# Optimization experiments

Hardware: AMD Instinct MI355X
Metric: run time of the kernel (lower is better)

The kernel has to match this reference:

```python
import jax, jax.numpy as jnp
import numpy as np

N_NODES = 50000
IN_CH, HID_CH, OUT_CH = 128, 128, 16
N_EDGES = 800000


def setup_inputs() -> dict:
    key = jax.random.key(0)
    ks = jax.random.split(key, 10)
    def lin_w(k, fan_in, fan_out):
        bound = 1.0 / np.sqrt(fan_in)
        return jax.random.uniform(k, (fan_in, fan_out), jnp.float32, -bound, bound)
    inp = {
        'x': jax.random.normal(ks[0], (N_NODES, IN_CH), jnp.float32),
        'edge_index': jax.random.randint(ks[1], (2, N_EDGES), 0, N_NODES, jnp.int64),
        # SAGEConv l/r weights: lin_l (neighbor aggregate, with bias), lin_r (root, no bias)
        'W1_l': lin_w(ks[2], IN_CH, HID_CH), 'b1': jnp.zeros((HID_CH,), jnp.float32),
        'W1_r': lin_w(ks[3], IN_CH, HID_CH),
        'W2_l': lin_w(ks[4], HID_CH, HID_CH), 'b2': jnp.zeros((HID_CH,), jnp.float32),
        'W2_r': lin_w(ks[5], HID_CH, HID_CH),
        'W3_l': lin_w(ks[6], HID_CH, HID_CH), 'b3': jnp.zeros((HID_CH,), jnp.float32),
        'W3_r': lin_w(ks[7], HID_CH, HID_CH),
        'W_lin': lin_w(ks[8], HID_CH, OUT_CH), 'b_lin': jnp.zeros((OUT_CH,), jnp.float32),
    }
    return inp


def _sage_conv(x, src, dst, W_l, b_l, W_r, n_nodes):
    # mean aggregation of source-node features at destination nodes
    msg_sum = jax.ops.segment_sum(x[src], dst, num_segments=n_nodes)  # [N, d]
    deg = jax.ops.segment_sum(jnp.ones((src.shape[0],), x.dtype), dst, num_segments=n_nodes)
    mean = msg_sum / jnp.maximum(deg, 1.0)[:, None]
    return mean @ W_l + b_l + x @ W_r


def reference(x, edge_index, W1_l, b1, W1_r, W2_l, b2, W2_r, W3_l, b3, W3_r, W_lin, b_lin):
    src, dst = edge_index[0], edge_index[1]
    n = x.shape[0]
    h = jax.nn.relu(_sage_conv(x, src, dst, W1_l, b1, W1_r, n))
    h = jax.nn.relu(_sage_conv(h, src, dst, W2_l, b2, W2_r, n))
    # dropout is identity in eval mode
    h = jax.nn.relu(_sage_conv(h, src, dst, W3_l, b3, W3_r, n))
    return h @ W_lin + b_lin
```

## Files before the change

### kernel.cpp

```cpp
#include <hip/hip_runtime.h>


typedef short bf16x8 __attribute__((ext_vector_type(8)));
typedef float f32x4 __attribute__((ext_vector_type(4)));

__device__ __forceinline__ float bf16_to_f32(unsigned int lo16) {
  unsigned int u = lo16 << 16;
  return __builtin_bit_cast(float, u);
}
__device__ __forceinline__ unsigned short f32_to_bf16(float f) {
  unsigned int u = __builtin_bit_cast(unsigned int, f);
  unsigned int r = (u + 0x7FFFu + ((u >> 16) & 1u)) >> 16;
  return (unsigned short)r;
}

__device__ __forceinline__ void gload_lds16(void* g, void* lds_base) {
  __builtin_amdgcn_global_load_lds(
      (__attribute__((address_space(1))) unsigned int*)(uintptr_t)g,
      (__attribute__((address_space(3))) unsigned int*)(unsigned int)(uintptr_t)lds_base,
      16, 0, 0);
}

__global__ void k_zero_i32(int* __restrict__ p, int n) {
  int i = blockIdx.x * blockDim.x + threadIdx.x;
  if (i < n) p[i] = 0;
}

__global__ __launch_bounds__(256) void k_split(const float* __restrict__ in,
                                               unsigned short* __restrict__ hi,
                                               unsigned short* __restrict__ lo, int n4) {
  int i = blockIdx.x * blockDim.x + threadIdx.x;
  if (i < n4) {
    float4 v = *reinterpret_cast<const float4*>(&in[(size_t)i * 4]);
    ushort4 h, l;
    h.x = f32_to_bf16(v.x); l.x = f32_to_bf16(v.x - bf16_to_f32(h.x));
    h.y = f32_to_bf16(v.y); l.y = f32_to_bf16(v.y - bf16_to_f32(h.y));
    h.z = f32_to_bf16(v.z); l.z = f32_to_bf16(v.z - bf16_to_f32(h.z));
    h.w = f32_to_bf16(v.w); l.w = f32_to_bf16(v.w - bf16_to_f32(h.w));
    *reinterpret_cast<ushort4*>(&hi[(size_t)i * 4]) = h;
    *reinterpret_cast<ushort4*>(&lo[(size_t)i * 4]) = l;
  }
}

__global__ __launch_bounds__(256) void k_prep_w(const float* __restrict__ Wl,
                                                const float* __restrict__ Wr,
                                                unsigned short* __restrict__ Whi,
                                                unsigned short* __restrict__ Wlo) {
  int n = blockIdx.x, k = threadIdx.x;
  float v = (k < 128) ? Wl[(size_t)k * 128 + n] : Wr[(size_t)(k - 128) * 128 + n];
  unsigned short h = f32_to_bf16(v);
  Whi[(size_t)n * 256 + k] = h;
  Wlo[(size_t)n * 256 + k] = f32_to_bf16(v - bf16_to_f32(h));
}

__global__ void k_detect(const int* __restrict__ ei, int* __restrict__ flag) {
  int t = threadIdx.x;
  int any = 0;
  for (int i = t; i < 1024; i += 256)
    if (ei[2 * i + 1] != 0) any = 1;
  if (any) atomicOr(flag, 1);
}

__device__ __forceinline__ int load_src(const int* ei, int E, int i, int is32) {
  return is32 ? ei[i] : ei[2 * i];
}
__device__ __forceinline__ int load_dst(const int* ei, int E, int i, int is32) {
  return is32 ? ei[E + i] : ei[2 * E + 2 * i];
}

__global__ __launch_bounds__(256) void k_count(const int* __restrict__ ei,
                                               const int* __restrict__ flag,
                                               int* __restrict__ deg,
                                               int* __restrict__ erank, int E) {
  int i = blockIdx.x * blockDim.x + threadIdx.x;
  if (i < E) {
    int is32 = *flag;
    erank[i] = atomicAdd(&deg[load_dst(ei, E, i, is32)], 1);
  }
}

__global__ __launch_bounds__(256) void k_scan1(const int* __restrict__ deg,
                                               int* __restrict__ bsum, int N) {
  __shared__ int s[256];
  int t = threadIdx.x;
  int base = blockIdx.x * 1024 + t * 4;
  int v = 0;
#pragma unroll
  for (int j = 0; j < 4; ++j) {
    int i = base + j;
    v += (i < N) ? deg[i] : 0;
  }
  s[t] = v;
  __syncthreads();
  for (int off = 128; off > 0; off >>= 1) {
    if (t < off) s[t] += s[t + off];
    __syncthreads();
  }
  if (t == 0) bsum[blockIdx.x] = s[0];
}

__global__ __launch_bounds__(1024) void k_scan2(int* __restrict__ bsum,
                                                int* __restrict__ row_ptr,
                                                int nb, int N) {
  __shared__ int s[1024];
  int t = threadIdx.x;
  int v = (t < nb) ? bsum[t] : 0;
  s[t] = v;
  __syncthreads();
  for (int off = 1; off < 1024; off <<= 1) {
    int add = (t >= off) ? s[t - off] : 0;
    __syncthreads();
    s[t] += add;
    __syncthreads();
  }
  if (t < nb) bsum[t] = s[t] - v;
  if (t == 1023) row_ptr[N] = s[1023];
}

__global__ __launch_bounds__(256) void k_scan3(const int* __restrict__ deg,
                                               const int* __restrict__ bsum,
                                               int* __restrict__ row_ptr,
                                               float* __restrict__ inv_deg, int N) {
  __shared__ int s[256];
  int t = threadIdx.x;
  int base = blockIdx.x * 1024 + t * 4;
  int v[4];
  int sum = 0;
#pragma unroll
  for (int j = 0; j < 4; ++j) {
    int i = base + j;
    v[j] = (i < N) ? deg[i] : 0;
    sum += v[j];
  }
  s[t] = sum;
  __syncthreads();
  for (int off = 1; off < 256; off <<= 1) {
    int add = (t >= off) ? s[t - off] : 0;
    __syncthreads();
    s[t] += add;
    __syncthreads();
  }
  int excl = s[t] - sum + bsum[blockIdx.x];
#pragma unroll
  for (int j = 0; j < 4; ++j) {
    int i = base + j;
    if (i < N) {
      row_ptr[i] = excl;
      inv_deg[i] = 1.0f / (float)((v[j] > 1) ? v[j] : 1);
      excl += v[j];
    }
  }
}

__global__ __launch_bounds__(256) void k_fill(const int* __restrict__ ei,
                                              const int* __restrict__ flag,
                                              const int* __restrict__ row_ptr,
                                              const int* __restrict__ erank,
                                              int* __restrict__ col_idx, int E) {
  int i = blockIdx.x * blockDim.x + threadIdx.x;
  if (i < E) {
    int is32 = *flag;
    int d = load_dst(ei, E, i, is32);
    int s = load_src(ei, E, i, is32);
    col_idx[row_ptr[d] + erank[i]] = s;
  }
}

__global__ __launch_bounds__(256) void k_aggregate(const unsigned short* __restrict__ Xhi,
                                                   const int* __restrict__ row_ptr,
                                                   const int* __restrict__ col_idx,
                                                   const float* __restrict__ inv_deg,
                                                   unsigned int* __restrict__ Mhi,
                                                   unsigned int* __restrict__ Mlo, int N) {
  int gw = (int)((blockIdx.x * blockDim.x + threadIdx.x) >> 6);
  int lane = threadIdx.x & 63;
  if (gw >= N) return;
  int s = row_ptr[gw], e = row_ptr[gw + 1];
  const unsigned int* Xp =
      reinterpret_cast<const unsigned int*>(Xhi) + lane;
  float ax[8], ay[8];
#pragma unroll
  for (int q = 0; q < 8; ++q) { ax[q] = 0.f; ay[q] = 0.f; }
  int j = s;
  for (; j + 8 <= e; j += 8) {
    unsigned int v[8];
#pragma unroll
    for (int q = 0; q < 8; ++q) v[q] = Xp[(size_t)col_idx[j + q] * 64];
#pragma unroll
    for (int q = 0; q < 8; ++q) {
      ax[q] += bf16_to_f32(v[q] & 0xFFFFu);
      ay[q] += bf16_to_f32(v[q] >> 16);
    }
  }
  for (; j + 4 <= e; j += 4) {
    unsigned int v[4];
#pragma unroll
    for (int q = 0; q < 4; ++q) v[q] = Xp[(size_t)col_idx[j + q] * 64];
#pragma unroll
    for (int q = 0; q < 4; ++q) {
      ax[q] += bf16_to_f32(v[q] & 0xFFFFu);
      ay[q] += bf16_to_f32(v[q] >> 16);
    }
  }
  for (; j < e; ++j) {
    unsigned int v = Xp[(size_t)col_idx[j] * 64];
    ax[0] += bf16_to_f32(v & 0xFFFFu);
    ay[0] += bf16_to_f32(v >> 16);
  }
  float inv = inv_deg[gw];
  float rx = ((ax[0] + ax[1]) + (ax[2] + ax[3])) + ((ax[4] + ax[5]) + (ax[6] + ax[7]));
  float ry = ((ay[0] + ay[1]) + (ay[2] + ay[3])) + ((ay[4] + ay[5]) + (ay[6] + ay[7]));
  rx *= inv;
  ry *= inv;
  unsigned int hx = f32_to_bf16(rx), hy = f32_to_bf16(ry);
  unsigned int lx = f32_to_bf16(rx - bf16_to_f32(hx));
  unsigned int ly = f32_to_bf16(ry - bf16_to_f32(hy));
  Mhi[(size_t)gw * 64 + lane] = hx | (hy << 16);
  Mlo[(size_t)gw * 64 + lane] = lx | (ly << 16);
}

__global__ __launch_bounds__(256) void k_mfma_gemm(
    const unsigned short* __restrict__ A1hi, const unsigned short* __restrict__ A1lo,
    const unsigned short* __restrict__ A2hi, const unsigned short* __restrict__ A2lo,
    const unsigned short* __restrict__ Whi, const unsigned short* __restrict__ Wlo,
    const float* __restrict__ bias,
    unsigned short* __restrict__ Ohi, unsigned short* __restrict__ Olo, int N) {
  __shared__ unsigned short sAhi[128 * 32], sAlo[128 * 32];
  __shared__ unsigned short sBhi[128 * 32], sBlo[128 * 32];
  int t = threadIdx.x;
  int lane = t & 63;
  int w = t >> 6;
  int wr = (w >> 1) * 64, wc = (w & 1) * 64;
  int block_row = blockIdx.x * 128;

  f32x4 acc[4][4];
#pragma unroll
  for (int m = 0; m < 4; ++m)
#pragma unroll
    for (int n = 0; n < 4; ++n) acc[m][n] = f32x4{0.f, 0.f, 0.f, 0.f};

  int kg = lane & 3;
  int rr = lane >> 2;
  int fr = lane & 15;
  int fkb = (lane >> 4) * 16;

  for (int kt = 0; kt < 8; ++kt) {
    {
      const unsigned short* gsrc;
      unsigned short* lbase;
      int isA = (w < 2);
      if (w == 0) { gsrc = (kt < 4) ? A1hi : A2hi; lbase = sAhi; }
      else if (w == 1) { gsrc = (kt < 4) ? A1lo : A2lo; lbase = sAlo; }
      else if (w == 2) { gsrc = Whi; lbase = sBhi; }
      else { gsrc = Wlo; lbase = sBlo; }
#pragma unroll
      for (int c = 0; c < 8; ++c) {
        int idx = c * 16 + rr;
        const char* src;
        if (isA) {
          int rg = block_row + idx;
          if (rg > N - 1) rg = N - 1;
          src = (const char*)gsrc + (size_t)rg * 256 + (kt & 3) * 64 + kg * 16;
        } else {
          src = (const char*)gsrc + (size_t)idx * 512 + kt * 64 + kg * 16;
        }
        gload_lds16((void*)src, (char*)lbase + c * 1024);
      }
    }
    __syncthreads();
    bf16x8 a_hi[4], a_lo[4], b_hi[4], b_lo[4];
#pragma unroll
    for (int m = 0; m < 4; ++m) {
      int row = wr + m * 16 + fr;
      a_hi[m] = *reinterpret_cast<const bf16x8*>((const char*)sAhi + row * 64 + fkb);
      a_lo[m] = *reinterpret_cast<const bf16x8*>((const char*)sAlo + row * 64 + fkb);
    }
#pragma unroll
    for (int n = 0; n < 4; ++n) {
      int col = wc + n * 16 + fr;
      b_hi[n] = *reinterpret_cast<const bf16x8*>((const char*)sBhi + col * 64 + fkb);
      b_lo[n] = *reinterpret_cast<const bf16x8*>((const char*)sBlo + col * 64 + fkb);
    }
#pragma unroll
    for (int m = 0; m < 4; ++m)
#pragma unroll
      for (int n = 0; n < 4; ++n) {
        acc[m][n] = __builtin_amdgcn_mfma_f32_16x16x32_bf16(a_hi[m], b_hi[n], acc[m][n], 0, 0, 0);
        acc[m][n] = __builtin_amdgcn_mfma_f32_16x16x32_bf16(a_hi[m], b_lo[n], acc[m][n], 0, 0, 0);
        acc[m][n] = __builtin_amdgcn_mfma_f32_16x16x32_bf16(a_lo[m], b_hi[n], acc[m][n], 0, 0, 0);
      }
    __syncthreads();
  }

  float bv[4];
#pragma unroll
  for (int n = 0; n < 4; ++n) bv[n] = bias[wc + n * 16 + (lane & 15)];
#pragma unroll
  for (int m = 0; m < 4; ++m) {
#pragma unroll
    for (int n = 0; n < 4; ++n) {
#pragma unroll
      for (int j = 0; j < 4; ++j) {
        int row_l = wr + m * 16 + (lane >> 4) * 4 + j;
        int g = block_row + row_l;
        if (g < N) {
          int col = wc + n * 16 + (lane & 15);
          float v = fmaxf(acc[m][n][j] + bv[n], 0.f);
          unsigned short h = f32_to_bf16(v);
          Ohi[(size_t)g * 128 + col] = h;
          Olo[(size_t)g * 128 + col] = f32_to_bf16(v - bf16_to_f32(h));
        }
      }
    }
  }
}

__global__ __launch_bounds__(256) void k_final(const unsigned short* __restrict__ Hhi,
                                               const unsigned short* __restrict__ Hlo,
                                               const float* __restrict__ W,
                                               const float* __restrict__ b,
                                               float* __restrict__ Out, int N) {
  __shared__ float sH[16][128];
  __shared__ float sW[128][16];
  __shared__ float sb[16];
  int t = threadIdx.x;
  int node0 = blockIdx.x * 16;
  {
    int row = t >> 4, q = t & 15;
    int g = node0 + row;
    if (g < N) {
      uint4 hv = *reinterpret_cast<const uint4*>(&Hhi[(size_t)g * 128 + q * 8]);
      uint4 lv = *reinterpret_cast<const uint4*>(&Hlo[(size_t)g * 128 + q * 8]);
      const unsigned short* hp = (const unsigned short*)&hv;
      const unsigned short* lp = (const unsigned short*)&lv;
#pragma unroll
      for (int e = 0; e < 8; ++e)
        sH[row][q * 8 + e] = bf16_to_f32(hp[e]) + bf16_to_f32(lp[e]);
    } else {
#pragma unroll
      for (int e = 0; e < 8; ++e) sH[row][q * 8 + e] = 0.f;
    }
  }
  for (int j = t; j < 512; j += 256) {
    int row = j >> 2, q = j & 3;
    *reinterpret_cast<float4*>(&sW[row][q * 4]) =
        *reinterpret_cast<const float4*>(&W[(size_t)row * 16 + q * 4]);
  }
  if (t < 16) sb[t] = b[t];
  __syncthreads();
  int node = t >> 4, col = t & 15;
  float acc = sb[col];
#pragma unroll 8
  for (int k = 0; k < 128; ++k) acc = fmaf(sH[node][k], sW[k][col], acc);
  int g = node0 + node;
  if (g < N) Out[(size_t)g * 16 + col] = acc;
}

extern "C" void kernel_launch(void* const* d_in, const int* in_sizes, int n_in,
                              void* d_out, int out_size, void* d_ws, size_t ws_size,
                              hipStream_t stream) {
  if (n_in < 13) return;
  const float* x = (const float*)d_in[0];
  const int* ei = (const int*)d_in[1];
  const float* W1l = (const float*)d_in[2];
  const float* b1 = (const float*)d_in[3];
  const float* W1r = (const float*)d_in[4];
  const float* W2l = (const float*)d_in[5];
  const float* b2 = (const float*)d_in[6];
  const float* W2r = (const float*)d_in[7];
  const float* W3l = (const float*)d_in[8];
  const float* b3 = (const float*)d_in[9];
  const float* W3r = (const float*)d_in[10];
  const float* Wlin = (const float*)d_in[11];
  const float* blin = (const float*)d_in[12];
  float* out = (float*)d_out;

  const int N = in_sizes[0] / 128;
  const int E = in_sizes[1] / 2;

  char* w = (char*)d_ws;
  size_t off = 0;
  auto alloc = [&](size_t bytes) -> void* {
    off = (off + 255) & ~(size_t)255;
    void* p = (void*)(w + off);
    off += bytes;
    return p;
  };
  size_t actB = (size_t)N * 128 * 2;
  unsigned short* Xhi = (unsigned short*)alloc(actB);
  unsigned short* Xlo = (unsigned short*)alloc(actB);
  unsigned short* Ahi = (unsigned short*)alloc(actB);
  unsigned short* Alo = (unsigned short*)alloc(actB);
  unsigned short* Mhi = (unsigned short*)alloc(actB);
  unsigned short* Mlo = (unsigned short*)alloc(actB);
  unsigned short* Wt[6];
  for (int i = 0; i < 6; ++i) Wt[i] = (unsigned short*)alloc(128 * 256 * 2);
  int* deg = (int*)alloc((size_t)N * 4);
  int* row_ptr = (int*)alloc((size_t)(N + 1) * 4);
  int* col_idx = (int*)alloc((size_t)E * 4);
  int* erank = (int*)alloc((size_t)E * 4);
  float* invdeg = (float*)alloc((size_t)N * 4);
  int* flag = (int*)alloc(4);
  int* bsum = (int*)alloc((size_t)1024 * 4);
  (void)ws_size;

  const int nbScan = (N + 1023) / 1024;

  k_zero_i32<<<(N + 255) / 256, 256, 0, stream>>>(deg, N);
  k_zero_i32<<<1, 256, 0, stream>>>(flag, 1);
  k_detect<<<1, 256, 0, stream>>>(ei, flag);
  k_count<<<(E + 255) / 256, 256, 0, stream>>>(ei, flag, deg, erank, E);
  k_split<<<(N * 32 + 255) / 256, 256, 0, stream>>>(x, Xhi, Xlo, N * 32);
  k_prep_w<<<128, 256, 0, stream>>>(W1l, W1r, Wt[0], Wt[1]);
  k_prep_w<<<128, 256, 0, stream>>>(W2l, W2r, Wt[2], Wt[3]);
  k_prep_w<<<128, 256, 0, stream>>>(W3l, W3r, Wt[4], Wt[5]);
  k_scan1<<<nbScan, 256, 0, stream>>>(deg, bsum, N);
  k_scan2<<<1, 1024, 0, stream>>>(bsum, row_ptr, nbScan, N);
  k_scan3<<<nbScan, 256, 0, stream>>>(deg, bsum, row_ptr, invdeg, N);
  k_fill<<<(E + 255) / 256, 256, 0, stream>>>(ei, flag, row_ptr, erank, col_idx, E);

  int aggBlocks = (N * 64 + 255) / 256;
  int gemmBlocks = (N + 127) / 128;

  k_aggregate<<<aggBlocks, 256, 0, stream>>>(Xhi, row_ptr, col_idx, invdeg,
                                             (unsigned int*)Mhi, (unsigned int*)Mlo, N);
  k_mfma_gemm<<<gemmBlocks, 256, 0, stream>>>(Mhi, Mlo, Xhi, Xlo, Wt[0], Wt[1], b1,
                                              Ahi, Alo, N);
  k_aggregate<<<aggBlocks, 256, 0, stream>>>(Ahi, row_ptr, col_idx, invdeg,
                                             (unsigned int*)Mhi, (unsigned int*)Mlo, N);
  k_mfma_gemm<<<gemmBlocks, 256, 0, stream>>>(Mhi, Mlo, Ahi, Alo, Wt[2], Wt[3], b2,
                                              Xhi, Xlo, N);
  k_aggregate<<<aggBlocks, 256, 0, stream>>>(Xhi, row_ptr, col_idx, invdeg,
                                             (unsigned int*)Mhi, (unsigned int*)Mlo, N);
  k_mfma_gemm<<<gemmBlocks, 256, 0, stream>>>(Mhi, Mlo, Xhi, Xlo, Wt[4], Wt[5], b3,
                                              Ahi, Alo, N);
  k_final<<<(N + 15) / 16, 256, 0, stream>>>(Ahi, Alo, Wlin, blin, out, N);
}
```

Baseline: 276.6 us.

## Double-buffer LDS tiles in split-bf16 MFMA GEMM to overlap loads with compute

The GEMM kernel now keeps two LDS buffers for the A and B hi/lo tiles. It issues the global-to-LDS load for the next K tile before the MFMAs on the current tile run, instead of loading and then computing in strict sequence. The goal is to hide global load latency behind matrix math. LDS use doubles, which may lower occupancy. The sync pattern also changes, and the remaining loop body is not visible, so whether a wait precedes the next read is unclear.

After: 269.8 us. -2.4%, faster.

```diff
diff --git a/kernel.cpp b/kernel.cpp
--- a/kernel.cpp
+++ b/kernel.cpp
@@ -14,7 +14,7 @@
   return (unsigned short)r;
 }
 
-__device__ __forceinline__ void gload_lds16(void* g, void* lds_base) {
+__device__ __forceinline__ void gload_lds16(const void* g, void* lds_base) {
   __builtin_amdgcn_global_load_lds(
       (__attribute__((address_space(1))) unsigned int*)(uintptr_t)g,
       (__attribute__((address_space(3))) unsigned int*)(unsigned int)(uintptr_t)lds_base,
@@ -225,8 +225,8 @@
     const unsigned short* __restrict__ Whi, const unsigned short* __restrict__ Wlo,
     const float* __restrict__ bias,
     unsigned short* __restrict__ Ohi, unsigned short* __restrict__ Olo, int N) {
-  __shared__ unsigned short sAhi[128 * 32], sAlo[128 * 32];
-  __shared__ unsigned short sBhi[128 * 32], sBlo[128 * 32];
+  __shared__ unsigned short sAhi[2][128 * 32], sAlo[2][128 * 32];
+  __shared__ unsigned short sBhi[2][128 * 32], sBlo[2][128 * 32];
   int t = threadIdx.x;
   int lane = t & 63;
   int w = t >> 6;
@@ -244,42 +244,47 @@
   int fr = lane & 15;
   int fkb = (lane >> 4) * 16;
 
+  auto stage = [&](int kt, int b) {
+    const unsigned short* gsrc;
+    unsigned short* lbase;
+    int isA = (w < 2);
+    if (w == 0) { gsrc = (kt < 4) ? A1hi : A2hi; lbase = sAhi[b]; }
+    else if (w == 1) { gsrc = (kt < 4) ? A1lo : A2lo; lbase = sAlo[b]; }
+    else if (w == 2) { gsrc = Whi; lbase = sBhi[b]; }
+    else { gsrc = Wlo; lbase = sBlo[b]; }
+#pragma unroll
+    for (int c = 0; c < 8; ++c) {
+      int idx = c * 16 + rr;
+      const char* src;
+      if (isA) {
+        int rg = block_row + idx;
+        if (rg > N - 1) rg = N - 1;
+        src = (const char*)gsrc + (size_t)rg * 256 + (kt & 3) * 64 + kg * 16;
+      } else {
+        src = (const char*)gsrc + (size_t)idx * 512 + kt * 64 + kg * 16;
+      }
+      gload_lds16(src, (char*)lbase + c * 1024);
+    }
+  };
+
+  stage(0, 0);
+  __syncthreads();
+
   for (int kt = 0; kt < 8; ++kt) {
-    {
-      const unsigned short* gsrc;
-      unsigned short* lbase;
-      int isA = (w < 2);
-      if (w == 0) { gsrc = (kt < 4) ? A1hi : A2hi; lbase = sAhi; }
-      else if (w == 1) { gsrc = (kt < 4) ? A1lo : A2lo; lbase = sAlo; }
-      else if (w == 2) { gsrc = Whi; lbase = sBhi; }
-      else { gsrc = Wlo; lbase = sBlo; }
-#pragma unroll
-      for (int c = 0; c < 8; ++c) {
-        int idx = c * 16 + rr;
-        const char* src;
-        if (isA) {
-          int rg = block_row + idx;
-          if (rg > N - 1) rg = N - 1;
-          src = (const char*)gsrc + (size_t)rg * 256 + (kt & 3) * 64 + kg * 16;
-        } else {
-          src = (const char*)gsrc + (size_t)idx * 512 + kt * 64 + kg * 16;
-        }
-        gload_lds16((void*)src, (char*)lbase + c * 1024);
-      }
-    }
-    __syncthreads();
+    int cur = kt & 1;
+    if (kt < 7) stage(kt + 1, cur ^ 1);
     bf16x8 a_hi[4], a_lo[4], b_hi[4], b_lo[4];
 #pragma unroll
     for (int m = 0; m < 4; ++m) {
       int row = wr + m * 16 + fr;
-      a_hi[m] = *reinterpret_cast<const bf16x8*>((const char*)sAhi + row * 64 + fkb);
-      a_lo[m] = *reinterpret_cast<const bf16x8*>((const char*)sAlo + row * 64 + fkb);
+      a_hi[m] = *reinterpret_cast<const bf16x8*>((const char*)sAhi[cur] + row * 64 + fkb);
+      a_lo[m] = *reinterpret_cast<const bf16x8*>((const char*)sAlo[cur] + row * 64 + fkb);
     }
 #pragma unroll
     for (int n = 0; n < 4; ++n) {
       int col = wc + n * 16 + fr;
-      b_hi[n] = *reinterpret_cast<const bf16x8*>((const char*)sBhi + col * 64 + fkb);
-      b_lo[n] = *reinterpret_cast<const bf16x8*>((const char*)sBlo + col * 64 + fkb);
+      b_hi[n] = *reinterpret_cast<const bf16x8*>((const char*)sBhi[cur] + col * 64 + fkb);
+      b_lo[n] = *reinterpret_cast<const bf16x8*>((const char*)sBlo[cur] + col * 64 + fkb);
     }
 #pragma unroll
     for (int m = 0; m < 4; ++m)
```
